# Kernel optimization log

Measured on AMD Instinct MI355X. Metric: run time of the kernel, lower is better.

The kernel has to match this reference:

```python
import jax, jax.numpy as jnp
import numpy as np

# ---- static config (matches init_kwargs / input_specs) ----
MODEL_CONTEXT_LEN = 4096
BLOCK_SIZE = 16
NUM_Q_HEADS = 32
NUM_KV_HEADS = 8
HEAD_DIM = 128
ROPE_BASE = 10000.0
B = 8
NUM_PAST = 4613                                   # context_len - 1, same for all seqs
END_BNUM = NUM_PAST // BLOCK_SIZE                 # 288
REM = NUM_PAST % BLOCK_SIZE                       # 5
START_BNUM = (NUM_PAST - MODEL_CONTEXT_LEN) // BLOCK_SIZE + 2  # 34
CUR_POS = MODEL_CONTEXT_LEN - 1                   # 4095 (capped decode position)
BLOCKS_PER_SEQ = END_BNUM + 1                     # 289
NUM_BLOCKS = B * BLOCKS_PER_SEQ                   # 2312


def rope(pos, x):
    """NeoX-style rotary. pos: [T] int; x: [..., T, H, D]."""
    half = HEAD_DIM // 2
    inv = 1.0 / (ROPE_BASE ** (jnp.arange(half, dtype=jnp.float32) / half))
    freqs = pos.astype(jnp.float32)[:, None] * inv        # [T, half]
    cos = jnp.cos(freqs)[:, None, :]                      # [T, 1, half]
    sin = jnp.sin(freqs)[:, None, :]
    x1, x2 = jnp.split(x, 2, axis=-1)
    return jnp.concatenate([x1 * cos - x2 * sin, x2 * cos + x1 * sin], axis=-1)


def setup_inputs() -> dict:
    key = jax.random.key(0)
    ks = jax.random.split(key, 7)
    q = jax.random.normal(ks[0], (B, NUM_Q_HEADS * HEAD_DIM), jnp.float32)
    k = jax.random.normal(ks[1], (B, NUM_KV_HEADS * HEAD_DIM), jnp.float32)
    v = jax.random.normal(ks[2], (B, NUM_KV_HEADS * HEAD_DIM), jnp.float32)
    positions = jnp.full((B,), NUM_PAST, dtype=jnp.int32)
    context_lens = jnp.full((B,), NUM_PAST + 1, dtype=jnp.int32)
    # distinct physical blocks per sequence (paged layout)
    block_tables = jnp.arange(NUM_BLOCKS, dtype=jnp.int32).reshape(B, BLOCKS_PER_SEQ)
    # cache stores UN-rotated keys (module writes k_original); layout [nblk, bs, Hk, D]
    key_cache = jax.random.normal(ks[3], (NUM_BLOCKS, BLOCK_SIZE, NUM_KV_HEADS, HEAD_DIM), jnp.float32) * 0.5
    value_cache = jax.random.normal(ks[4], (NUM_BLOCKS, BLOCK_SIZE, NUM_KV_HEADS, HEAD_DIM), jnp.float32) * 0.5
    W_o = jax.random.normal(ks[5], (NUM_Q_HEADS * HEAD_DIM, NUM_Q_HEADS * HEAD_DIM), jnp.float32) * 0.02
    return {"q": q, "k": k, "v": v, "positions": positions, "context_lens": context_lens,
            "block_tables": block_tables, "key_cache": key_cache, "value_cache": value_cache, "W_o": W_o}


def reference(q, k, v, positions, context_lens, block_tables, key_cache, value_cache, W_o):
    # Decode path of StreamingAttentionSink, context > model_context_len:
    # gather sink block + sliding-window blocks, re-apply rotary at shifted
    # positions, attend with q/k roped at capped position, project output.
    # positions for re-roped past keys: sink tokens 0..bs-1, window tokens
    # 2*bs-1-rem .. model_context_len-2 (matches the torch code's pos arange).
    pos_sink = np.arange(BLOCK_SIZE)
    pos_win = np.arange(2 * BLOCK_SIZE - 1 - REM, MODEL_CONTEXT_LEN - 1)
    POS = jnp.asarray(np.concatenate([pos_sink, pos_win]), dtype=jnp.int32)  # [4085]

    qh = q.reshape(B, NUM_Q_HEADS, HEAD_DIM)
    kh = k.reshape(B, NUM_KV_HEADS, HEAD_DIM)
    vh = v.reshape(B, NUM_KV_HEADS, HEAD_DIM)

    # phys_bnums = [block_table[0]] + block_table[start:end]  -> [B, 255]
    phys = jnp.concatenate([block_tables[:, :1], block_tables[:, START_BNUM:END_BNUM]], axis=1)
    full_k = key_cache[phys].reshape(B, -1, NUM_KV_HEADS, HEAD_DIM)       # [B, 4080, Hk, D]
    rem_k = key_cache[block_tables[:, END_BNUM], :REM]                     # [B, 5, Hk, D]
    past_k = jnp.concatenate([full_k, rem_k], axis=1)                      # [B, 4085, Hk, D]
    full_v = value_cache[phys].reshape(B, -1, NUM_KV_HEADS, HEAD_DIM)
    rem_v = value_cache[block_tables[:, END_BNUM], :REM]
    past_v = jnp.concatenate([full_v, rem_v], axis=1)

    past_k = rope(POS, past_k)  # re-apply rotary to shifted sink/window keys

    cur = jnp.array([CUR_POS], dtype=jnp.int32)
    q_rot = rope(cur, qh[:, None, :, :])[:, 0]   # [B, H, D] at capped position
    k_rot = rope(cur, kh[:, None, :, :])[:, 0]   # [B, Hk, D]

    keys = jnp.concatenate([past_k, k_rot[:, None]], axis=1)   # [B, 4086, Hk, D]
    vals = jnp.concatenate([past_v, vh[:, None]], axis=1)

    # GQA attention (group = 4 q-heads per kv-head)
    G = NUM_Q_HEADS // NUM_KV_HEADS
    qg = q_rot.reshape(B, NUM_KV_HEADS, G, HEAD_DIM)
    scale = 1.0 / np.sqrt(HEAD_DIM).astype(np.float32)
    scores = jnp.einsum('bhgd,bthd->bhgt', qg, keys) * scale
    probs = jax.nn.softmax(scores, axis=-1)
    attn = jnp.einsum('bhgt,bthd->bhgd', probs, vals).reshape(B, NUM_Q_HEADS * HEAD_DIM)
    return attn @ W_o
```

## Files before the change

### kernel.cpp

```cpp
#include <hip/hip_runtime.h>
#include <math.h>

#define NB 8
#define NQH 32
#define NKVH 8
#define HD 128
#define GQ 4
#define T_TOT 4086
#define SPLITS 32
#define TCHUNK 128
#define TILE 32
#define PPAD 130
#define BPS 289
#define LOG2_10K_OVER_64 0.2076205059304601f
#define SCALE 0.08838834764831843f

#define PART_ATTN_OFF 0
#define PART_ATTN_SZ  (64 * GQ * SPLITS * PPAD)
#define ATTN_OFF      PART_ATTN_SZ
#define PART_GEMM_OFF 0

__device__ __forceinline__ void rope_cs(float posf, int j, float& cs, float& sn)
{
    const float INV2PI = 0.15915494309189535f;
    const float P1 = 6.28125f;
    const float P2 = 0.0019354820251464844f;
    const float P3 = -1.748455600075e-7f;
    float inv  = __builtin_amdgcn_exp2f(-(float)j * LOG2_10K_OVER_64);
    float freq = posf * inv;
    float n    = rintf(freq * INV2PI);
    float red  = fmaf(-n, P1, freq);
    red        = fmaf(-n, P2, red);
    red        = fmaf(-n, P3, red);
    float rev  = red * INV2PI;
    sn = __builtin_amdgcn_sinf(rev);
    cs = __builtin_amdgcn_cosf(rev);
}

__global__ __launch_bounds__(256) void attn_partial_kernel(
    const float* __restrict__ q, const float* __restrict__ k, const float* __restrict__ v,
    const int* __restrict__ bt, const float* __restrict__ kc, const float* __restrict__ vc,
    float* __restrict__ part)
{
    __shared__ float kt[TILE][132];
    __shared__ float vt[TILE][128];
    __shared__ float qs[GQ][132];
    __shared__ float sc[GQ][36];
    __shared__ unsigned int offr[TCHUNK];
    __shared__ int posr[TCHUNK];
    __shared__ float lred[4][GQ];

    const int tid  = threadIdx.x;
    const int bh   = blockIdx.x;
    const int s    = blockIdx.y;
    const int b    = bh >> 3, h = bh & 7;
    const int lane = tid & 63, w = tid >> 6;
    const int t0   = s * TCHUNK;
    const int* btb = bt + b * BPS;

    if (tid < TCHUNK) {
        int tg = t0 + tid;
        unsigned int off; int pos;
        if (tg == T_TOT - 1)      { off = 0xFFFFFFFFu; pos = 4095; }
        else if (tg < T_TOT - 1) {
            int bti, rr;
            if (tg < 16)        { bti = 0;              rr = tg;        pos = tg;      }
            else if (tg < 4080) { bti = 33 + (tg >> 4); rr = tg & 15;   pos = tg + 10; }
            else                { bti = 288;            rr = tg - 4080; pos = tg + 10; }
            off = (unsigned int)(((btb[bti] * 16 + rr) * NKVH + h) * HD);
        } else                    { off = 0u; pos = 0; }
        offr[tid] = off; posr[tid] = pos;
    }
    {
        const float* qp = q + (size_t)b * (NQH * HD) + (size_t)h * (GQ * HD);
        for (int e = tid; e < GQ * HD; e += 256) {
            int g = e >> 7, d = e & 127, j = d & 63;
            float cs, sn; rope_cs(4095.0f, j, cs, sn);
            float x1 = qp[g * HD + j], x2 = qp[g * HD + j + 64];
            qs[g][d] = ((d < 64) ? (x1 * cs - x2 * sn) : (x2 * cs + x1 * sn)) * SCALE;
        }
    }

    float acc0 = 0.f, acc1 = 0.f, l_run = 0.f;
    const int g_s = (lane >> 4) & 3, tl_s = (lane >> 1) & 7, hf = lane & 1;
    const int gp = w >> 1, cc = (w & 1) * 64 + lane;

    for (int tb = 0; tb < TCHUNK; tb += TILE) {
        __syncthreads();

        #pragma unroll
        for (int it = 0; it < 2; ++it) {
            int e = tid + it * 256;
            int row = e >> 4, c4 = (e & 15) << 2;
            unsigned int off = offr[tb + row];
            float posf = (float)posr[tb + row];
            const float* ks = (off == 0xFFFFFFFFu) ? (k + (size_t)(b * NKVH + h) * HD)
                                                   : (kc + off);
            float4 k1 = *(const float4*)(ks + c4);
            float4 k2 = *(const float4*)(ks + 64 + c4);
            float4 lo, hi; float cs, sn;
            rope_cs(posf, c4 + 0, cs, sn); lo.x = k1.x*cs - k2.x*sn; hi.x = k2.x*cs + k1.x*sn;
            rope_cs(posf, c4 + 1, cs, sn); lo.y = k1.y*cs - k2.y*sn; hi.y = k2.y*cs + k1.y*sn;
            rope_cs(posf, c4 + 2, cs, sn); lo.z = k1.z*cs - k2.z*sn; hi.z = k2.z*cs + k1.z*sn;
            rope_cs(posf, c4 + 3, cs, sn); lo.w = k1.w*cs - k2.w*sn; hi.w = k2.w*cs + k1.w*sn;
            *(float4*)&kt[row][c4]      = lo;
            *(float4*)&kt[row][64 + c4] = hi;
        }
        #pragma unroll
        for (int it = 0; it < 4; ++it) {
            int e = tid + it * 256;
            int row = e >> 5, c4 = (e & 31) << 2;
            unsigned int off = offr[tb + row];
            const float* vs = (off == 0xFFFFFFFFu) ? (v + (size_t)(b * NKVH + h) * HD)
                                                   : (vc + off);
            *(float4*)&vt[row][c4] = *(const float4*)(vs + c4);
        }
        __syncthreads();

        {
            int t = w * 8 + tl_s;
            const float* kr = &kt[t][hf * 64];
            const float* qr = &qs[g_s][hf * 64];
            float dot = 0.f;
            #pragma unroll
            for (int j4 = 0; j4 < 16; ++j4) {
                float4 kk = *(const float4*)(kr + (j4 << 2));
                float4 qq = *(const float4*)(qr + (j4 << 2));
                dot += kk.x*qq.x + kk.y*qq.y + kk.z*qq.z + kk.w*qq.w;
            }
            dot += __shfl_xor(dot, 1);
            int tg = t0 + tb + t;
            float p = (tg < T_TOT) ? __builtin_amdgcn_exp2f(dot * 1.4426950408889634f) : 0.f;
            l_run += p;
            if (hf == 0) sc[g_s][t] = p;
        }
        __syncthreads();

        #pragma unroll
        for (int t4 = 0; t4 < 8; ++t4) {
            float4 p40 = *(const float4*)&sc[2*gp][t4 << 2];
            float4 p41 = *(const float4*)&sc[2*gp + 1][t4 << 2];
            int t = t4 << 2;
            float v0 = vt[t][cc], v1 = vt[t+1][cc], v2 = vt[t+2][cc], v3 = vt[t+3][cc];
            acc0 += p40.x*v0 + p40.y*v1 + p40.z*v2 + p40.w*v3;
            acc1 += p41.x*v0 + p41.y*v1 + p41.z*v2 + p41.w*v3;
        }
    }

    float lr = l_run;
    lr += __shfl_xor(lr, 1); lr += __shfl_xor(lr, 2);
    lr += __shfl_xor(lr, 4); lr += __shfl_xor(lr, 8);
    if ((lane & 15) == 0) lred[w][lane >> 4] = lr;
    __syncthreads();

    float* pp0 = part + ((size_t)(bh * GQ + 2*gp    ) * SPLITS + s) * PPAD;
    float* pp1 = part + ((size_t)(bh * GQ + 2*gp + 1) * SPLITS + s) * PPAD;
    pp0[cc] = acc0;
    pp1[cc] = acc1;
    if (tid < GQ) {
        float l = 0.5f * (lred[0][tid] + lred[1][tid] + lred[2][tid] + lred[3][tid]);
        part[((size_t)(bh * GQ + tid) * SPLITS + s) * PPAD + 129] = l;
    }
}

__global__ __launch_bounds__(256) void attn_reduce_kernel(
    const float* __restrict__ part, float* __restrict__ attn)
{
    int bh = blockIdx.x;
    int tid = threadIdx.x;
    int g = tid >> 6, lane = tid & 63;
    const float* pg = part + (size_t)(bh * GQ + g) * SPLITS * PPAD;
    float accl = 0.f, acch = 0.f, l = 0.f;
    #pragma unroll 8
    for (int s = 0; s < SPLITS; ++s) {
        l    += pg[s * PPAD + 129];
        accl += pg[s * PPAD + lane];
        acch += pg[s * PPAD + lane + 64];
    }
    int b = bh >> 3, h = bh & 7;
    float inv_l = 1.0f / l;
    size_t base = (size_t)b * 4096 + (size_t)(h * GQ + g) * 128;
    attn[base + lane]      = accl * inv_l;
    attn[base + lane + 64] = acch * inv_l;
}

__global__ __launch_bounds__(256) void gemm_partial_kernel(
    const float* __restrict__ attn, const float* __restrict__ Wo,
    float* __restrict__ part)
{
    __shared__ float a_s[NB][256];
    __shared__ float red[4][NB][128];
    int tid = threadIdx.x;
    int lane = tid & 63, w = tid >> 6;
    int jt = blockIdx.x;
    int is = blockIdx.y;
    int i0 = is * 256;
    int c  = jt * 128 + lane * 2;
    for (int e = tid; e < NB * 256; e += 256) {
        int bb = e >> 8, i = e & 255;
        a_s[bb][i] = attn[(size_t)bb * 4096 + i0 + i];
    }
    __syncthreads();
    float accx[NB] = {}, accy[NB] = {};
    const float* wp = Wo + (size_t)(i0 + w * 64) * 4096 + c;
    #pragma unroll 8
    for (int ii = 0; ii < 64; ++ii) {
        float2 wv = *(const float2*)(wp + (size_t)ii * 4096);
        int il = w * 64 + ii;
        #pragma unroll
        for (int bb = 0; bb < NB; ++bb) {
            float a = a_s[bb][il];
            accx[bb] += a * wv.x;
            accy[bb] += a * wv.y;
        }
    }
    #pragma unroll
    for (int bb = 0; bb < NB; ++bb) {
        red[w][bb][lane * 2]     = accx[bb];
        red[w][bb][lane * 2 + 1] = accy[bb];
    }
    __syncthreads();
    for (int e = tid; e < NB * 128; e += 256) {
        int bb = e >> 7, l = e & 127;
        float sum = red[0][bb][l] + red[1][bb][l] + red[2][bb][l] + red[3][bb][l];
        part[(size_t)is * 32768 + (size_t)bb * 4096 + jt * 128 + l] = sum;
    }
}

__global__ __launch_bounds__(256) void gemm_reduce_kernel(
    const float* __restrict__ part, float* __restrict__ out)
{
    int idx = blockIdx.x * 256 + threadIdx.x;
    float4 sum = {0.f, 0.f, 0.f, 0.f};
    #pragma unroll
    for (int s = 0; s < 16; ++s) {
        float4 p = *(const float4*)(part + (size_t)s * 32768 + (size_t)idx * 4);
        sum.x += p.x; sum.y += p.y; sum.z += p.z; sum.w += p.w;
    }
    *(float4*)(out + (size_t)idx * 4) = sum;
}

extern "C" void kernel_launch(void* const* d_in, const int* in_sizes, int n_in,
                              void* d_out, int out_size, void* d_ws, size_t ws_size,
                              hipStream_t stream) {
    const float* q  = (const float*)d_in[0];
    const float* k  = (const float*)d_in[1];
    const float* v  = (const float*)d_in[2];
    const int*   bt = (const int*)d_in[5];
    const float* kc = (const float*)d_in[6];
    const float* vc = (const float*)d_in[7];
    const float* Wo = (const float*)d_in[8];
    float* out = (float*)d_out;
    float* ws  = (float*)d_ws;

    float* part_attn = ws + PART_ATTN_OFF;
    float* attn      = ws + ATTN_OFF;
    float* part_gemm = ws + PART_GEMM_OFF;

    attn_partial_kernel<<<dim3(64, SPLITS), 256, 0, stream>>>(q, k, v, bt, kc, vc, part_attn);
    attn_reduce_kernel<<<64, 256, 0, stream>>>(part_attn, attn);
    gemm_partial_kernel<<<dim3(32, 16), 256, 0, stream>>>(attn, Wo, part_gemm);
    gemm_reduce_kernel<<<32, 256, 0, stream>>>(part_gemm, out);
}
```

Before: 361.7 us.

## Move current-token attention into reduce, read V directly, atomically accumulate GEMM output

The current token's key/value contribution is now computed in the reduce kernel, so the partial kernel loops only over cached tokens and drops the per-row branch between new and cached K/V. V is read from global memory straight into the PV accumulation instead of being staged in shared memory, which removes one tile load and cuts LDS use. The partial kernel also gets a launch-bounds occupancy hint. The GEMM split-K reduce kernel is removed: the output is zeroed in the attention reduce kernel and partials are added with atomicAdd, saving one launch at the cost of atomic traffic and non-deterministic summation order.

```diff
diff --git a/kernel.cpp b/kernel.cpp
--- a/kernel.cpp
+++ b/kernel.cpp
@@ -7,6 +7,7 @@
 #define HD 128
 #define GQ 4
 #define T_TOT 4086
+#define T_PAST 4085
 #define SPLITS 32
 #define TCHUNK 128
 #define TILE 32
@@ -14,11 +15,11 @@
 #define BPS 289
 #define LOG2_10K_OVER_64 0.2076205059304601f
 #define SCALE 0.08838834764831843f
+#define LOG2E 1.4426950408889634f
 
 #define PART_ATTN_OFF 0
 #define PART_ATTN_SZ  (64 * GQ * SPLITS * PPAD)
 #define ATTN_OFF      PART_ATTN_SZ
-#define PART_GEMM_OFF 0
 
 __device__ __forceinline__ void rope_cs(float posf, int j, float& cs, float& sn)
 {
@@ -37,13 +38,12 @@
     cs = __builtin_amdgcn_cosf(rev);
 }
 
-__global__ __launch_bounds__(256) void attn_partial_kernel(
-    const float* __restrict__ q, const float* __restrict__ k, const float* __restrict__ v,
+__global__ __launch_bounds__(256, 6) void attn_partial_kernel(
+    const float* __restrict__ q,
     const int* __restrict__ bt, const float* __restrict__ kc, const float* __restrict__ vc,
     float* __restrict__ part)
 {
     __shared__ float kt[TILE][132];
-    __shared__ float vt[TILE][128];
     __shared__ float qs[GQ][132];
     __shared__ float sc[GQ][36];
     __shared__ unsigned int offr[TCHUNK];
@@ -60,15 +60,14 @@
 
     if (tid < TCHUNK) {
         int tg = t0 + tid;
-        unsigned int off; int pos;
-        if (tg == T_TOT - 1)      { off = 0xFFFFFFFFu; pos = 4095; }
-        else if (tg < T_TOT - 1) {
+        unsigned int off = 0u; int pos = 0;
+        if (tg < T_PAST) {
             int bti, rr;
             if (tg < 16)        { bti = 0;              rr = tg;        pos = tg;      }
             else if (tg < 4080) { bti = 33 + (tg >> 4); rr = tg & 15;   pos = tg + 10; }
             else                { bti = 288;            rr = tg - 4080; pos = tg + 10; }
             off = (unsigned int)(((btb[bti] * 16 + rr) * NKVH + h) * HD);
-        } else                    { off = 0u; pos = 0; }
+        }
         offr[tid] = off; posr[tid] = pos;
     }
     {
@@ -84,6 +83,7 @@
     float acc0 = 0.f, acc1 = 0.f, l_run = 0.f;
     const int g_s = (lane >> 4) & 3, tl_s = (lane >> 1) & 7, hf = lane & 1;
     const int gp = w >> 1, cc = (w & 1) * 64 + lane;
+    const float* vcc = vc + cc;
 
     for (int tb = 0; tb < TCHUNK; tb += TILE) {
         __syncthreads();
@@ -94,8 +94,7 @@
             int row = e >> 4, c4 = (e & 15) << 2;
             unsigned int off = offr[tb + row];
             float posf = (float)posr[tb + row];
-            const float* ks = (off == 0xFFFFFFFFu) ? (k + (size_t)(b * NKVH + h) * HD)
-                                                   : (kc + off);
+            const float* ks = kc + off;
             float4 k1 = *(const float4*)(ks + c4);
             float4 k2 = *(const float4*)(ks + 64 + c4);
             float4 lo, hi; float cs, sn;
@@ -105,15 +104,6 @@
             rope_cs(posf, c4 + 3, cs, sn); lo.w = k1.w*cs - k2.w*sn; hi.w = k2.w*cs + k1.w*sn;
             *(float4*)&kt[row][c4]      = lo;
             *(float4*)&kt[row][64 + c4] = hi;
-        }
-        #pragma unroll
-        for (int it = 0; it < 4; ++it) {
-            int e = tid + it * 256;
-            int row = e >> 5, c4 = (e & 31) << 2;
-            unsigned int off = offr[tb + row];
-            const float* vs = (off == 0xFFFFFFFFu) ? (v + (size_t)(b * NKVH + h) * HD)
-                                                   : (vc + off);
-            *(float4*)&vt[row][c4] = *(const float4*)(vs + c4);
         }
         __syncthreads();
 
@@ -130,7 +120,7 @@
             }
             dot += __shfl_xor(dot, 1);
             int tg = t0 + tb + t;
-            float p = (tg < T_TOT) ? __builtin_amdgcn_exp2f(dot * 1.4426950408889634f) : 0.f;
+            float p = (tg < T_PAST) ? __builtin_amdgcn_exp2f(dot * LOG2E) : 0.f;
             l_run += p;
             if (hf == 0) sc[g_s][t] = p;
         }
@@ -141,7 +131,10 @@
             float4 p40 = *(const float4*)&sc[2*gp][t4 << 2];
             float4 p41 = *(const float4*)&sc[2*gp + 1][t4 << 2];
             int t = t4 << 2;
-            float v0 = vt[t][cc], v1 = vt[t+1][cc], v2 = vt[t+2][cc], v3 = vt[t+3][cc];
+            float v0 = vcc[offr[tb + t]];
+            float v1 = vcc[offr[tb + t + 1]];
+            float v2 = vcc[offr[tb + t + 2]];
+            float v3 = vcc[offr[tb + t + 3]];
             acc0 += p40.x*v0 + p40.y*v1 + p40.z*v2 + p40.w*v3;
             acc1 += p41.x*v0 + p41.y*v1 + p41.z*v2 + p41.w*v3;
         }
@@ -164,11 +157,30 @@
 }
 
 __global__ __launch_bounds__(256) void attn_reduce_kernel(
-    const float* __restrict__ part, float* __restrict__ attn)
+    const float* __restrict__ part,
+    const float* __restrict__ q, const float* __restrict__ k, const float* __restrict__ v,
+    float* __restrict__ attn, float* __restrict__ out)
 {
     int bh = blockIdx.x;
     int tid = threadIdx.x;
     int g = tid >> 6, lane = tid & 63;
+    int b = bh >> 3, h = bh & 7;
+
+    *(float2*)(out + (size_t)(bh * 256 + tid) * 2) = make_float2(0.f, 0.f);
+
+    const float* qp = q + (size_t)b * (NQH * HD) + (size_t)(h * GQ + g) * HD;
+    const float* kp = k + (size_t)(b * NKVH + h) * HD;
+    float cs, sn; rope_cs(4095.0f, lane, cs, sn);
+    float q1 = qp[lane], q2 = qp[lane + 64];
+    float k1 = kp[lane], k2 = kp[lane + 64];
+    float qr1 = q1*cs - q2*sn, qr2 = q2*cs + q1*sn;
+    float kr1 = k1*cs - k2*sn, kr2 = k2*cs + k1*sn;
+    float dot = qr1*kr1 + qr2*kr2;
+    dot += __shfl_xor(dot, 1);  dot += __shfl_xor(dot, 2);
+    dot += __shfl_xor(dot, 4);  dot += __shfl_xor(dot, 8);
+    dot += __shfl_xor(dot, 16); dot += __shfl_xor(dot, 32);
+    float p_cur = __builtin_amdgcn_exp2f(dot * SCALE * LOG2E);
+
     const float* pg = part + (size_t)(bh * GQ + g) * SPLITS * PPAD;
     float accl = 0.f, acch = 0.f, l = 0.f;
     #pragma unroll 8
@@ -177,7 +189,10 @@
         accl += pg[s * PPAD + lane];
         acch += pg[s * PPAD + lane + 64];
     }
-    int b = bh >> 3, h = bh & 7;
+    const float* vp = v + (size_t)(b * NKVH + h) * HD;
+    accl += p_cur * vp[lane];
+    acch += p_cur * vp[lane + 64];
+    l += p_cur;
     float inv_l = 1.0f / l;
     size_t base = (size_t)b * 4096 + (size_t)(h * GQ + g) * 128;
     attn[base + lane]      = accl * inv_l;
@@ -186,7 +201,7 @@
 
 __global__ __launch_bounds__(256) void gemm_partial_kernel(
     const float* __restrict__ attn, const float* __restrict__ Wo,
-    float* __restrict__ part)
+    float* __restrict__ out)
 {
     __shared__ float a_s[NB][256];
     __shared__ float red[4][NB][128];
@@ -223,21 +238,8 @@
     for (int e = tid; e < NB * 128; e += 256) {
         int bb = e >> 7, l = e & 127;
         float sum = red[0][bb][l] + red[1][bb][l] + red[2][bb][l] + red[3][bb][l];
-        part[(size_t)is * 32768 + (size_t)bb * 4096 + jt * 128 + l] = sum;
-    }
-}
-
-__global__ __launch_bounds__(256) void gemm_reduce_kernel(
-    const float* __restrict__ part, float* __restrict__ out)
-{
-    int idx = blockIdx.x * 256 + threadIdx.x;
-    float4 sum = {0.f, 0.f, 0.f, 0.f};
-    #pragma unroll
-    for (int s = 0; s < 16; ++s) {
-        float4 p = *(const float4*)(part + (size_t)s * 32768 + (size_t)idx * 4);
-        sum.x += p.x; sum.y += p.y; sum.z += p.z; sum.w += p.w;
-    }
-    *(float4*)(out + (size_t)idx * 4) = sum;
+        atomicAdd(&out[(size_t)bb * 4096 + jt * 128 + l], sum);
+    }
 }
 
 extern "C" void kernel_launch(void* const* d_in, const int* in_sizes, int n_in,
@@ -255,10 +257,8 @@
 
     float* part_attn = ws + PART_ATTN_OFF;
     float* attn      = ws + ATTN_OFF;
-    float* part_gemm = ws + PART_GEMM_OFF;
-
-    attn_partial_kernel<<<dim3(64, SPLITS), 256, 0, stream>>>(q, k, v, bt, kc, vc, part_attn);
-    attn_reduce_kernel<<<64, 256, 0, stream>>>(part_attn, attn);
-    gemm_partial_kernel<<<dim3(32, 16), 256, 0, stream>>>(attn, Wo, part_gemm);
-    gemm_reduce_kernel<<<32, 256, 0, stream>>>(part_gemm, out);
-}
+
+    attn_partial_kernel<<<dim3(64, SPLITS), 256, 0, stream>>>(q, bt, kc, vc, part_attn);
+    attn_reduce_kernel<<<64, 256, 0, stream>>>(part_attn, q, k, v, attn, out);
+    gemm_partial_kernel<<<dim3(32, 16), 256, 0, stream>>>(attn, Wo, out);
+}
```

Result: slower. 377.9 us (+4.5%).
